# Kernel optimization log

Measured on AMD Instinct MI355X. Metric: run time of the kernel, lower is better.

The kernel has to match this reference:

```python
import jax, jax.numpy as jnp
import numpy as np

IN_CH, OUT_CH, K, N = 32, 64, 7, 64  # input_channels, output_channels, kernel_size, input_size


def _pad_kernel(kernel):
    # Replicates OpticalConv2dNew.process_inputs/__pad for K < N:
    # symmetric pad by (N-K)//2, then (0,1,0,1) if size still off by one.
    p = (N - K) // 2
    extra = 1 if (K + 2 * p) != N else 0
    return jnp.pad(kernel, ((0, 0), (0, 0), (p, p + extra), (p, p + extra)))


def _opt_conv(img, ker):
    # Ideal 4f optical convolution (FFT-based, circular): |fftshift(ifft2(fft2(ifftshift(x)) * fft2(ifftshift(h))))|
    ax = (-2, -1)
    F = jnp.fft.fft2(jnp.fft.ifftshift(img, axes=ax))      # (B,1,in,N,N) complex
    G = jnp.fft.fft2(jnp.fft.ifftshift(ker, axes=ax))      # (1,out,in,N,N) complex
    out = jnp.fft.fftshift(jnp.fft.ifft2(F * G), axes=ax)  # (B,out,in,N,N)
    return jnp.abs(out)


def setup_inputs() -> dict:
    key = jax.random.key(0)
    k1, k2 = jax.random.split(key)
    B = 8
    inputs = {
        "input": jax.random.normal(k1, (B, IN_CH, N, N), dtype=jnp.float32),
        # kaiming-uniform-like init for the learned kernel parameter
        "kernel": jax.random.uniform(k2, (OUT_CH, IN_CH, K, K), dtype=jnp.float32,
                                     minval=-1.0, maxval=1.0) * float(np.sqrt(6.0 / (IN_CH * K * K))),
    }
    return inputs


def reference(input, kernel):
    ker = _pad_kernel(kernel)                 # (out,in,N,N)
    img = input[:, None, :, :, :]             # (B,1,in,N,N) — broadcast instead of repeat/reshape
    ker = ker[None, :, :, :, :]               # (1,out,in,N,N)
    out = _opt_conv(img, ker)                 # (B,out,in,N,N) float32 (abs of complex)
    return jnp.sum(out, axis=2)               # sum over input channels -> (B,out,N,N)
```

## Files before the change

kernel.cpp:

```cpp
#include <hip/hip_runtime.h>

typedef __attribute__((ext_vector_type(8))) short short8;
typedef __attribute__((ext_vector_type(4))) float f32x4;

namespace {

__device__ __forceinline__ unsigned short f2bf(float f) {
    unsigned int u = __float_as_uint(f);
    u += 0x7fffu + ((u >> 16) & 1u);
    return (unsigned short)(u >> 16);
}

__global__ void prep_B(const float* __restrict__ ker, uint4* __restrict__ B2) {
    int t  = blockIdx.x * 256 + threadIdx.x;
    int a  = t & 7;
    int oc = (t >> 3) & 63;
    int ic = t >> 9;
    unsigned int d[4] = {0u, 0u, 0u, 0u};
    if (a < 7) {
        const float* row = ker + ((oc * 32 + ic) * 49) + (6 - a) * 7;
        float v[8];
#pragma unroll
        for (int q = 0; q < 7; ++q) v[q] = row[6 - q];
        v[7] = 0.0f;
#pragma unroll
        for (int j = 0; j < 4; ++j)
            d[j] = (unsigned int)f2bf(v[2 * j]) | ((unsigned int)f2bf(v[2 * j + 1]) << 16);
    }
    int nt = oc >> 4, n = oc & 15, ts = a >> 2, g = a & 3;
    B2[(ic * 8 + nt * 2 + ts) * 64 + g * 16 + n] = make_uint4(d[0], d[1], d[2], d[3]);
}

__global__ __launch_bounds__(512, 4) void conv_mfma(
    const float* __restrict__ img,
    const uint4* __restrict__ B2,
    float* __restrict__ out)
{
    __shared__ unsigned int H[18000];

    const int bid  = blockIdx.x;
    const int y    = bid & 63;
    const int b    = bid >> 6;
    const int tid  = threadIdx.x;
    const int lane = tid & 63;
    const int w    = tid >> 6;
    const int xh   = w & 1;
    const int icg  = w >> 1;
    const int n    = lane & 15;
    const int g    = lane >> 4;

    const float* base = img + (size_t)b * 32 * 4096;

    float v[28];
#pragma unroll
    for (int j = 0; j < 28; ++j) {
        const int pl  = 4 * w + j / 7;
        const int row = (y - 2 + (j % 7)) & 63;
        v[j] = base[pl * 4096 + row * 64 + lane];
    }
#pragma unroll
    for (int j = 0; j < 28; ++j) {
        const int pl = 4 * w + j / 7;
        const int r  = j % 7;
        const unsigned int h  = f2bf(v[j]);
        const unsigned int hn = (unsigned int)__shfl((int)h, (lane + 1) & 63);
        const unsigned int dw = h | (hn << 16);
        const int idx = pl * 560 + r * 80;
        H[idx + lane + 2] = dw;
        if (lane >= 62) H[idx + lane - 62] = dw;
        if (lane <= 5)  H[idx + lane + 66] = dw;
    }
    __syncthreads();

    f32x4 acc[2][4];
#pragma unroll
    for (int mt = 0; mt < 2; ++mt)
#pragma unroll
        for (int nt = 0; nt < 4; ++nt) acc[mt][nt] = (f32x4){0.f, 0.f, 0.f, 0.f};

    const int ic0 = icg * 8;
#pragma unroll 2
    for (int ici = 0; ici < 8; ++ici) {
        const int ic = ic0 + ici;
        uint4 bf[8];
#pragma unroll
        for (int q = 0; q < 8; ++q)
            bf[q] = B2[(ic * 8 + q) * 64 + lane];

#pragma unroll
        for (int mt = 0; mt < 2; ++mt) {
            const int x0 = 32 * xh + 16 * mt;
            const int b0 = ic * 560 + g * 80 + x0 + n;
            const int b1 = b0 + 320;
            uint4 i0 = make_uint4(H[b0], H[b0 + 2], H[b0 + 4], H[b0 + 6]);
            uint4 i1 = make_uint4(H[b1], H[b1 + 2], H[b1 + 4], H[b1 + 6]);
            short8 f0 = __builtin_bit_cast(short8, i0);
            short8 f1 = __builtin_bit_cast(short8, i1);
#pragma unroll
            for (int nt = 0; nt < 4; ++nt) {
                f32x4 d = (f32x4){0.f, 0.f, 0.f, 0.f};
                d = __builtin_amdgcn_mfma_f32_16x16x32_bf16(
                        __builtin_bit_cast(short8, bf[2 * nt]),     f0, d, 0, 0, 0);
                d = __builtin_amdgcn_mfma_f32_16x16x32_bf16(
                        __builtin_bit_cast(short8, bf[2 * nt + 1]), f1, d, 0, 0, 0);
#pragma unroll
                for (int i = 0; i < 4; ++i)
                    acc[mt][nt][i] += __builtin_fabsf(d[i]);
            }
        }
    }

    __syncthreads();
    float* P = (float*)H;
    if (icg & 1) {
        float* R = P + (icg >> 1) * 4160;
#pragma unroll
        for (int mt = 0; mt < 2; ++mt)
#pragma unroll
            for (int nt = 0; nt < 4; ++nt)
#pragma unroll
                for (int i = 0; i < 4; ++i)
                    R[(16 * nt + 4 * g + i) * 65 + 32 * xh + 16 * mt + n] = acc[mt][nt][i];
    }
    __syncthreads();
    if (icg == 0 || icg == 2) {
        float* R = P + (icg >> 1) * 4160;
#pragma unroll
        for (int mt = 0; mt < 2; ++mt)
#pragma unroll
            for (int nt = 0; nt < 4; ++nt)
#pragma unroll
                for (int i = 0; i < 4; ++i)
                    acc[mt][nt][i] += R[(16 * nt + 4 * g + i) * 65 + 32 * xh + 16 * mt + n];
    }
    if (icg == 2) {
        float* R = P + 4160;
#pragma unroll
        for (int mt = 0; mt < 2; ++mt)
#pragma unroll
            for (int nt = 0; nt < 4; ++nt)
#pragma unroll
                for (int i = 0; i < 4; ++i)
                    R[(16 * nt + 4 * g + i) * 65 + 32 * xh + 16 * mt + n] = acc[mt][nt][i];
    }
    __syncthreads();
    if (icg == 0) {
        float* R = P + 4160;
        float* o = out + (size_t)b * 64 * 4096 + y * 64;
#pragma unroll
        for (int mt = 0; mt < 2; ++mt) {
            const int x0 = 32 * xh + 16 * mt;
#pragma unroll
            for (int nt = 0; nt < 4; ++nt)
#pragma unroll
                for (int i = 0; i < 4; ++i) {
                    const int oc = 16 * nt + 4 * g + i;
                    o[(size_t)oc * 4096 + x0 + n] =
                        acc[mt][nt][i] + R[oc * 65 + x0 + n];
                }
        }
    }
}

}

extern "C" void kernel_launch(void* const* d_in, const int* in_sizes, int n_in,
                              void* d_out, int out_size, void* d_ws, size_t ws_size,
                              hipStream_t stream) {
    const float* img = (const float*)d_in[0];
    const float* ker = (const float*)d_in[1];
    float* out = (float*)d_out;
    uint4* B2 = (uint4*)d_ws;

    prep_B<<<dim3(64), dim3(256), 0, stream>>>(ker, B2);
    conv_mfma<<<dim3(512), dim3(512), 0, stream>>>(img, B2, out);
}
```

Baseline: 74.62 us.

## Process two output rows per block with 1024 threads and tree reduction

Each block now computes two output rows instead of one, using 16 waves (1024 threads) where each wave handles 4 input channels, and the halo rows are shared between the two rows. This cuts redundant image loads and weight fragment loads per output row, and halves the grid to 256 blocks. The cross-wave reduction becomes a multi-stage LDS tree with more syncthreads, and the larger accumulator arrays raise register pressure, which may reduce occupancy.

```diff
diff --git a/kernel.cpp b/kernel.cpp
--- a/kernel.cpp
+++ b/kernel.cpp
@@ -27,20 +27,21 @@
         for (int j = 0; j < 4; ++j)
             d[j] = (unsigned int)f2bf(v[2 * j]) | ((unsigned int)f2bf(v[2 * j + 1]) << 16);
     }
-    int nt = oc >> 4, n = oc & 15, ts = a >> 2, g = a & 3;
-    B2[(ic * 8 + nt * 2 + ts) * 64 + g * 16 + n] = make_uint4(d[0], d[1], d[2], d[3]);
-}
-
-__global__ __launch_bounds__(512, 4) void conv_mfma(
+    int ot = oc >> 4, n = oc & 15, kt = a >> 2, g = a & 3;
+    B2[(ic * 8 + ot * 2 + kt) * 64 + g * 16 + n] = make_uint4(d[0], d[1], d[2], d[3]);
+}
+
+__global__ __launch_bounds__(1024, 4) void conv_mfma(
     const float* __restrict__ img,
     const uint4* __restrict__ B2,
     float* __restrict__ out)
 {
-    __shared__ unsigned int H[18000];
+    __shared__ unsigned int H[18576];
 
     const int bid  = blockIdx.x;
-    const int y    = bid & 63;
-    const int b    = bid >> 6;
+    const int yp   = bid & 31;
+    const int b    = bid >> 5;
+    const int y0   = yp * 2;
     const int tid  = threadIdx.x;
     const int lane = tid & 63;
     const int w    = tid >> 6;
@@ -51,112 +52,146 @@
 
     const float* base = img + (size_t)b * 32 * 4096;
 
-    float v[28];
-#pragma unroll
-    for (int j = 0; j < 28; ++j) {
-        const int pl  = 4 * w + j / 7;
-        const int row = (y - 2 + (j % 7)) & 63;
+    if (tid < 144) H[18432 + tid] = 0u;
+
+    float v[16];
+#pragma unroll
+    for (int j = 0; j < 16; ++j) {
+        const int pl  = 2 * w + (j >> 3);
+        const int row = (y0 - 2 + (j & 7)) & 63;
         v[j] = base[pl * 4096 + row * 64 + lane];
     }
 #pragma unroll
-    for (int j = 0; j < 28; ++j) {
-        const int pl = 4 * w + j / 7;
-        const int r  = j % 7;
+    for (int j = 0; j < 16; ++j) {
+        const int pl = 2 * w + (j >> 3);
+        const int r  = j & 7;
         const unsigned int h  = f2bf(v[j]);
         const unsigned int hn = (unsigned int)__shfl((int)h, (lane + 1) & 63);
         const unsigned int dw = h | (hn << 16);
-        const int idx = pl * 560 + r * 80;
+        const int idx = pl * 576 + r * 72;
         H[idx + lane + 2] = dw;
         if (lane >= 62) H[idx + lane - 62] = dw;
         if (lane <= 5)  H[idx + lane + 66] = dw;
     }
     __syncthreads();
 
-    f32x4 acc[2][4];
-#pragma unroll
-    for (int mt = 0; mt < 2; ++mt)
-#pragma unroll
-        for (int nt = 0; nt < 4; ++nt) acc[mt][nt] = (f32x4){0.f, 0.f, 0.f, 0.f};
-
-    const int ic0 = icg * 8;
-#pragma unroll 2
-    for (int ici = 0; ici < 8; ++ici) {
-        const int ic = ic0 + ici;
+    f32x4 acc[4][4];
+#pragma unroll
+    for (int nt = 0; nt < 4; ++nt)
+#pragma unroll
+        for (int ot = 0; ot < 4; ++ot) acc[nt][ot] = (f32x4){0.f, 0.f, 0.f, 0.f};
+
+#pragma unroll 1
+    for (int ici = 0; ici < 4; ++ici) {
+        const int ic = icg * 4 + ici;
         uint4 bf[8];
 #pragma unroll
         for (int q = 0; q < 8; ++q)
             bf[q] = B2[(ic * 8 + q) * 64 + lane];
 
 #pragma unroll
-        for (int mt = 0; mt < 2; ++mt) {
-            const int x0 = 32 * xh + 16 * mt;
-            const int b0 = ic * 560 + g * 80 + x0 + n;
-            const int b1 = b0 + 320;
+        for (int nt = 0; nt < 4; ++nt) {
+            const int b0 = ic * 576 + ((nt >> 1) + g) * 72 + 32 * xh + 16 * (nt & 1) + n;
+            const int b1 = b0 + 288;
             uint4 i0 = make_uint4(H[b0], H[b0 + 2], H[b0 + 4], H[b0 + 6]);
             uint4 i1 = make_uint4(H[b1], H[b1 + 2], H[b1 + 4], H[b1 + 6]);
             short8 f0 = __builtin_bit_cast(short8, i0);
             short8 f1 = __builtin_bit_cast(short8, i1);
 #pragma unroll
-            for (int nt = 0; nt < 4; ++nt) {
+            for (int ot = 0; ot < 4; ++ot) {
                 f32x4 d = (f32x4){0.f, 0.f, 0.f, 0.f};
                 d = __builtin_amdgcn_mfma_f32_16x16x32_bf16(
-                        __builtin_bit_cast(short8, bf[2 * nt]),     f0, d, 0, 0, 0);
+                        __builtin_bit_cast(short8, bf[2 * ot]),     f0, d, 0, 0, 0);
                 d = __builtin_amdgcn_mfma_f32_16x16x32_bf16(
-                        __builtin_bit_cast(short8, bf[2 * nt + 1]), f1, d, 0, 0, 0);
-#pragma unroll
-                for (int i = 0; i < 4; ++i)
-                    acc[mt][nt][i] += __builtin_fabsf(d[i]);
+                        __builtin_bit_cast(short8, bf[2 * ot + 1]), f1, d, 0, 0, 0);
+#pragma unroll
+                for (int i = 0; i < 4; ++i)
+                    acc[nt][ot][i] += __builtin_fabsf(d[i]);
             }
         }
     }
 
-    __syncthreads();
     float* P = (float*)H;
-    if (icg & 1) {
-        float* R = P + (icg >> 1) * 4160;
-#pragma unroll
-        for (int mt = 0; mt < 2; ++mt)
-#pragma unroll
-            for (int nt = 0; nt < 4; ++nt)
-#pragma unroll
-                for (int i = 0; i < 4; ++i)
-                    R[(16 * nt + 4 * g + i) * 65 + 32 * xh + 16 * mt + n] = acc[mt][nt][i];
-    }
-    __syncthreads();
-    if (icg == 0 || icg == 2) {
-        float* R = P + (icg >> 1) * 4160;
-#pragma unroll
-        for (int mt = 0; mt < 2; ++mt)
-#pragma unroll
-            for (int nt = 0; nt < 4; ++nt)
-#pragma unroll
-                for (int i = 0; i < 4; ++i)
-                    acc[mt][nt][i] += R[(16 * nt + 4 * g + i) * 65 + 32 * xh + 16 * mt + n];
-    }
-    if (icg == 2) {
-        float* R = P + 4160;
-#pragma unroll
-        for (int mt = 0; mt < 2; ++mt)
-#pragma unroll
-            for (int nt = 0; nt < 4; ++nt)
-#pragma unroll
-                for (int i = 0; i < 4; ++i)
-                    R[(16 * nt + 4 * g + i) * 65 + 32 * xh + 16 * mt + n] = acc[mt][nt][i];
+    __syncthreads();
+
+#pragma unroll
+    for (int ph = 0; ph < 2; ++ph) {
+        if (icg >= 4) {
+            const int rb = ((icg - 4) * 2 + xh) * 2048;
+#pragma unroll
+            for (int nh = 0; nh < 2; ++nh) {
+                const int nt = 2 * ph + nh;
+                float* q = P + rb + (nh * 4 + 0) * 256 + lane * 4;
+#pragma unroll
+                for (int ot = 0; ot < 4; ++ot)
+#pragma unroll
+                    for (int i = 0; i < 4; ++i)
+                        P[rb + (nh * 4 + ot) * 256 + lane * 4 + i] = acc[nt][ot][i];
+                (void)q;
+            }
+        }
+        __syncthreads();
+        if (icg < 4) {
+            const int rb = (icg * 2 + xh) * 2048;
+#pragma unroll
+            for (int nh = 0; nh < 2; ++nh) {
+                const int nt = 2 * ph + nh;
+#pragma unroll
+                for (int ot = 0; ot < 4; ++ot)
+#pragma unroll
+                    for (int i = 0; i < 4; ++i)
+                        acc[nt][ot][i] += P[rb + (nh * 4 + ot) * 256 + lane * 4 + i];
+            }
+        }
+        __syncthreads();
+    }
+    if (icg == 2 || icg == 3) {
+        const int rb = ((icg - 2) * 2 + xh) * 4096;
+#pragma unroll
+        for (int nt = 0; nt < 4; ++nt)
+#pragma unroll
+            for (int ot = 0; ot < 4; ++ot)
+#pragma unroll
+                for (int i = 0; i < 4; ++i)
+                    P[rb + (nt * 4 + ot) * 256 + lane * 4 + i] = acc[nt][ot][i];
+    }
+    __syncthreads();
+    if (icg == 0 || icg == 1) {
+        const int rb = (icg * 2 + xh) * 4096;
+#pragma unroll
+        for (int nt = 0; nt < 4; ++nt)
+#pragma unroll
+            for (int ot = 0; ot < 4; ++ot)
+#pragma unroll
+                for (int i = 0; i < 4; ++i)
+                    acc[nt][ot][i] += P[rb + (nt * 4 + ot) * 256 + lane * 4 + i];
+    }
+    __syncthreads();
+    if (icg == 1) {
+        const int rb = xh * 4096;
+#pragma unroll
+        for (int nt = 0; nt < 4; ++nt)
+#pragma unroll
+            for (int ot = 0; ot < 4; ++ot)
+#pragma unroll
+                for (int i = 0; i < 4; ++i)
+                    P[rb + (nt * 4 + ot) * 256 + lane * 4 + i] = acc[nt][ot][i];
     }
     __syncthreads();
     if (icg == 0) {
-        float* R = P + 4160;
-        float* o = out + (size_t)b * 64 * 4096 + y * 64;
-#pragma unroll
-        for (int mt = 0; mt < 2; ++mt) {
-            const int x0 = 32 * xh + 16 * mt;
-#pragma unroll
-            for (int nt = 0; nt < 4; ++nt)
+        const int rb = xh * 4096;
+        float* o = out + (size_t)b * 64 * 4096;
+#pragma unroll
+        for (int nt = 0; nt < 4; ++nt) {
+            const int y  = y0 + (nt >> 1);
+            const int x0 = 32 * xh + 16 * (nt & 1);
+#pragma unroll
+            for (int ot = 0; ot < 4; ++ot)
 #pragma unroll
                 for (int i = 0; i < 4; ++i) {
-                    const int oc = 16 * nt + 4 * g + i;
-                    o[(size_t)oc * 4096 + x0 + n] =
-                        acc[mt][nt][i] + R[oc * 65 + x0 + n];
+                    const int oc = 16 * ot + 4 * g + i;
+                    o[(size_t)oc * 4096 + y * 64 + x0 + n] =
+                        acc[nt][ot][i] + P[rb + (nt * 4 + ot) * 256 + lane * 4 + i];
                 }
         }
     }
@@ -173,5 +208,5 @@
     uint4* B2 = (uint4*)d_ws;
 
     prep_B<<<dim3(64), dim3(256), 0, stream>>>(ker, B2);
-    conv_mfma<<<dim3(512), dim3(512), 0, stream>>>(img, B2, out);
-}
+    conv_mfma<<<dim3(256), dim3(1024), 0, stream>>>(img, B2, out);
+}
```

Result: no change. 74.21 us (-0.6%).

## Switch conv MFMA from 16x16x32 to 32x32x16 bf16 tiles with new weight layout

Applied to the files above, without the earlier changes.

Replaces the 16x16x32 bf16 MFMA tiling with 32x32x16 bf16 instructions, so each wave computes two 32-oc by 32-x tiles over four K-slices. prep_B now writes weights in a lane-linear layout that matches the new A-operand fragments, and the LDS row pitch shrinks from 80 to 72. The cross-wave reduction goes through float4-vectorized LDS writes. This cuts the MFMA instruction count and the number of abs/accumulate passes, at the cost of larger accumulator vectors and changed LDS bank patterns.

```diff
diff --git a/kernel.cpp b/kernel.cpp
--- a/kernel.cpp
+++ b/kernel.cpp
@@ -1,7 +1,7 @@
 #include <hip/hip_runtime.h>
 
-typedef __attribute__((ext_vector_type(8))) short short8;
-typedef __attribute__((ext_vector_type(4))) float f32x4;
+typedef __attribute__((ext_vector_type(8)))  short short8;
+typedef __attribute__((ext_vector_type(16))) float f32x16;
 
 namespace {
 
@@ -11,11 +11,22 @@
     return (unsigned short)(u >> 16);
 }
 
-__global__ void prep_B(const float* __restrict__ ker, uint4* __restrict__ B2) {
-    int t  = blockIdx.x * 256 + threadIdx.x;
-    int a  = t & 7;
-    int oc = (t >> 3) & 63;
-    int ic = t >> 9;
+__device__ __forceinline__ f32x16 zero16() {
+    f32x16 z;
+#pragma unroll
+    for (int r = 0; r < 16; ++r) z[r] = 0.0f;
+    return z;
+}
+
+__global__ void prep_B(const float* __restrict__ ker, uint4* __restrict__ B3) {
+    int t    = blockIdx.x * 256 + threadIdx.x;
+    int lane = t & 63;
+    int kq   = (t >> 6) & 3;
+    int ot   = (t >> 8) & 1;
+    int ic   = t >> 9;
+    int m = lane & 31, h = lane >> 5;
+    int oc = ot * 32 + m;
+    int a  = 2 * kq + h;
     unsigned int d[4] = {0u, 0u, 0u, 0u};
     if (a < 7) {
         const float* row = ker + ((oc * 32 + ic) * 49) + (6 - a) * 7;
@@ -27,16 +38,15 @@
         for (int j = 0; j < 4; ++j)
             d[j] = (unsigned int)f2bf(v[2 * j]) | ((unsigned int)f2bf(v[2 * j + 1]) << 16);
     }
-    int nt = oc >> 4, n = oc & 15, ts = a >> 2, g = a & 3;
-    B2[(ic * 8 + nt * 2 + ts) * 64 + g * 16 + n] = make_uint4(d[0], d[1], d[2], d[3]);
+    B3[t] = make_uint4(d[0], d[1], d[2], d[3]);
 }
 
 __global__ __launch_bounds__(512, 4) void conv_mfma(
     const float* __restrict__ img,
-    const uint4* __restrict__ B2,
+    const uint4* __restrict__ B3,
     float* __restrict__ out)
 {
-    __shared__ unsigned int H[18000];
+    __shared__ unsigned int H[16128];
 
     const int bid  = blockIdx.x;
     const int y    = bid & 63;
@@ -46,8 +56,8 @@
     const int w    = tid >> 6;
     const int xh   = w & 1;
     const int icg  = w >> 1;
-    const int n    = lane & 15;
-    const int g    = lane >> 4;
+    const int n31  = lane & 31;
+    const int h    = lane >> 5;
 
     const float* base = img + (size_t)b * 32 * 4096;
 
@@ -62,103 +72,93 @@
     for (int j = 0; j < 28; ++j) {
         const int pl = 4 * w + j / 7;
         const int r  = j % 7;
-        const unsigned int h  = f2bf(v[j]);
-        const unsigned int hn = (unsigned int)__shfl((int)h, (lane + 1) & 63);
-        const unsigned int dw = h | (hn << 16);
-        const int idx = pl * 560 + r * 80;
+        const unsigned int hh = f2bf(v[j]);
+        const unsigned int hn = (unsigned int)__shfl((int)hh, (lane + 1) & 63);
+        const unsigned int dw = hh | (hn << 16);
+        const int idx = pl * 504 + r * 72;
         H[idx + lane + 2] = dw;
         if (lane >= 62) H[idx + lane - 62] = dw;
         if (lane <= 5)  H[idx + lane + 66] = dw;
     }
     __syncthreads();
 
-    f32x4 acc[2][4];
-#pragma unroll
-    for (int mt = 0; mt < 2; ++mt)
-#pragma unroll
-        for (int nt = 0; nt < 4; ++nt) acc[mt][nt] = (f32x4){0.f, 0.f, 0.f, 0.f};
+    f32x16 acc[2] = {zero16(), zero16()};
+    const int xloc = 32 * xh + n31;
+    const int hv   = h * 72;
 
-    const int ic0 = icg * 8;
 #pragma unroll 2
     for (int ici = 0; ici < 8; ++ici) {
-        const int ic = ic0 + ici;
-        uint4 bf[8];
+        const int ic = icg * 8 + ici;
+        uint4 tf[8];
 #pragma unroll
         for (int q = 0; q < 8; ++q)
-            bf[q] = B2[(ic * 8 + q) * 64 + lane];
+            tf[q] = B3[ic * 512 + q * 64 + lane];
 
+        short8 fr[4];
 #pragma unroll
-        for (int mt = 0; mt < 2; ++mt) {
-            const int x0 = 32 * xh + 16 * mt;
-            const int b0 = ic * 560 + g * 80 + x0 + n;
-            const int b1 = b0 + 320;
-            uint4 i0 = make_uint4(H[b0], H[b0 + 2], H[b0 + 4], H[b0 + 6]);
-            uint4 i1 = make_uint4(H[b1], H[b1 + 2], H[b1 + 4], H[b1 + 6]);
-            short8 f0 = __builtin_bit_cast(short8, i0);
-            short8 f1 = __builtin_bit_cast(short8, i1);
+        for (int kq = 0; kq < 4; ++kq) {
+            const int ad = ic * 504 + ((kq < 3) ? (2 * kq * 72 + hv) : 432) + xloc;
+            uint4 t4 = make_uint4(H[ad], H[ad + 2], H[ad + 4], H[ad + 6]);
+            fr[kq] = __builtin_bit_cast(short8, t4);
+        }
 #pragma unroll
-            for (int nt = 0; nt < 4; ++nt) {
-                f32x4 d = (f32x4){0.f, 0.f, 0.f, 0.f};
-                d = __builtin_amdgcn_mfma_f32_16x16x32_bf16(
-                        __builtin_bit_cast(short8, bf[2 * nt]),     f0, d, 0, 0, 0);
-                d = __builtin_amdgcn_mfma_f32_16x16x32_bf16(
-                        __builtin_bit_cast(short8, bf[2 * nt + 1]), f1, d, 0, 0, 0);
+        for (int ot = 0; ot < 2; ++ot) {
+            f32x16 d = zero16();
 #pragma unroll
-                for (int i = 0; i < 4; ++i)
-                    acc[mt][nt][i] += __builtin_fabsf(d[i]);
-            }
+            for (int kq = 0; kq < 4; ++kq)
+                d = __builtin_amdgcn_mfma_f32_32x32x16_bf16(
+                        __builtin_bit_cast(short8, tf[ot * 4 + kq]), fr[kq], d, 0, 0, 0);
+#pragma unroll
+            for (int r = 0; r < 16; ++r)
+                acc[ot][r] += __builtin_fabsf(d[r]);
         }
     }
 
+    float* P = (float*)H;
     __syncthreads();
-    float* P = (float*)H;
     if (icg & 1) {
-        float* R = P + (icg >> 1) * 4160;
+        const int rb = ((icg >> 1) * 2 + xh) * 2048;
 #pragma unroll
-        for (int mt = 0; mt < 2; ++mt)
+        for (int ot = 0; ot < 2; ++ot)
 #pragma unroll
-            for (int nt = 0; nt < 4; ++nt)
+            for (int rq = 0; rq < 4; ++rq)
+                *(float4*)&P[rb + (ot * 4 + rq) * 256 + lane * 4] =
+                    make_float4(acc[ot][rq * 4], acc[ot][rq * 4 + 1],
+                                acc[ot][rq * 4 + 2], acc[ot][rq * 4 + 3]);
+    }
+    __syncthreads();
+    if (!(icg & 1)) {
+        const int rb = ((icg >> 1) * 2 + xh) * 2048;
+#pragma unroll
+        for (int ot = 0; ot < 2; ++ot)
+#pragma unroll
+            for (int rq = 0; rq < 4; ++rq)
 #pragma unroll
                 for (int i = 0; i < 4; ++i)
-                    R[(16 * nt + 4 * g + i) * 65 + 32 * xh + 16 * mt + n] = acc[mt][nt][i];
-    }
-    __syncthreads();
-    if (icg == 0 || icg == 2) {
-        float* R = P + (icg >> 1) * 4160;
-#pragma unroll
-        for (int mt = 0; mt < 2; ++mt)
-#pragma unroll
-            for (int nt = 0; nt < 4; ++nt)
-#pragma unroll
-                for (int i = 0; i < 4; ++i)
-                    acc[mt][nt][i] += R[(16 * nt + 4 * g + i) * 65 + 32 * xh + 16 * mt + n];
+                    acc[ot][rq * 4 + i] += P[rb + (ot * 4 + rq) * 256 + lane * 4 + i];
     }
     if (icg == 2) {
-        float* R = P + 4160;
+        const int rb = (4 + xh) * 2048;
 #pragma unroll
-        for (int mt = 0; mt < 2; ++mt)
+        for (int ot = 0; ot < 2; ++ot)
 #pragma unroll
-            for (int nt = 0; nt < 4; ++nt)
-#pragma unroll
-                for (int i = 0; i < 4; ++i)
-                    R[(16 * nt + 4 * g + i) * 65 + 32 * xh + 16 * mt + n] = acc[mt][nt][i];
+            for (int rq = 0; rq < 4; ++rq)
+                *(float4*)&P[rb + (ot * 4 + rq) * 256 + lane * 4] =
+                    make_float4(acc[ot][rq * 4], acc[ot][rq * 4 + 1],
+                                acc[ot][rq * 4 + 2], acc[ot][rq * 4 + 3]);
     }
     __syncthreads();
     if (icg == 0) {
-        float* R = P + 4160;
-        float* o = out + (size_t)b * 64 * 4096 + y * 64;
+        const int rb = (4 + xh) * 2048;
 #pragma unroll
-        for (int mt = 0; mt < 2; ++mt) {
-            const int x0 = 32 * xh + 16 * mt;
+        for (int ot = 0; ot < 2; ++ot)
 #pragma unroll
-            for (int nt = 0; nt < 4; ++nt)
-#pragma unroll
-                for (int i = 0; i < 4; ++i) {
-                    const int oc = 16 * nt + 4 * g + i;
-                    o[(size_t)oc * 4096 + x0 + n] =
-                        acc[mt][nt][i] + R[oc * 65 + x0 + n];
-                }
-        }
+            for (int reg = 0; reg < 16; ++reg) {
+                const int oc = 32 * ot + (reg & 3) + 8 * (reg >> 2) + 4 * h;
+                out[(size_t)(b * 64 + oc) * 4096 + y * 64 + xloc] =
+                    acc[ot][reg] +
+                    P[rb + (ot * 4 + (reg >> 2)) * 256 + lane * 4 + (reg & 3)];
+            }
     }
 }
 
@@ -170,8 +170,8 @@
     const float* img = (const float*)d_in[0];
     const float* ker = (const float*)d_in[1];
     float* out = (float*)d_out;
-    uint4* B2 = (uint4*)d_ws;
+    uint4* B3 = (uint4*)d_ws;
 
-    prep_B<<<dim3(64), dim3(256), 0, stream>>>(ker, B2);
-    conv_mfma<<<dim3(512), dim3(512), 0, stream>>>(img, B2, out);
+    prep_B<<<dim3(64), dim3(256), 0, stream>>>(ker, B3);
+    conv_mfma<<<dim3(512), dim3(512), 0, stream>>>(img, B3, out);
 }
```

Result: no change. 75.05 us (+0.6%).
